# Kernel tuning notes

Measured on AMD Instinct MI355X. Metric: run time of the kernel, lower is better.

## Reference

```python
import jax, jax.numpy as jnp
import numpy as np

V, S, D, H, L, F = 32000, 1024, 1024, 16, 6, 4096
DH = D // H          # 64
HALF = DH // 2       # 32
EPS = 1e-5
ROPE_BASE = 10000.0


def setup_inputs() -> dict:
    key = jax.random.key(0)
    ks = jax.random.split(key, 16)
    std = 0.02
    inp = {
        "tokens": jax.random.randint(ks[0], (4, S), 0, V),
        "tok_emb": jax.random.normal(ks[1], (V, D), jnp.float32) * std,
        "ln1_s": jnp.ones((L, D), jnp.float32),
        "ln1_b": jnp.zeros((L, D), jnp.float32),
        "w_qkv": jax.random.normal(ks[2], (L, D, 3 * D), jnp.float32) * std,
        "w_proj": jax.random.normal(ks[3], (L, D, D), jnp.float32) * std,
        "ln2_s": jnp.ones((L, D), jnp.float32),
        "ln2_b": jnp.zeros((L, D), jnp.float32),
        "w_in": jax.random.normal(ks[4], (L, D, 2 * F), jnp.float32) * std,
        "w_out": jax.random.normal(ks[5], (L, F, D), jnp.float32) * std,
        "lnf_s": jnp.ones((D,), jnp.float32),
        "lnf_b": jnp.zeros((D,), jnp.float32),
        "w_score": jax.random.normal(ks[6], (D, 1), jnp.float32) * std,
        "w_cls": jax.random.normal(ks[7], (D, S), jnp.float32) * std,
    }
    return inp


def _layernorm(x, s, b):
    m = x.mean(-1, keepdims=True)
    v = ((x - m) ** 2).mean(-1, keepdims=True)
    return (x - m) * jax.lax.rsqrt(v + EPS) * s + b


def _rotate_half(x):
    x_even = x[..., ::2]
    x_odd = x[..., 1::2]
    return jnp.stack((-x_odd, x_even), axis=-1).reshape(x.shape)


def _rope_tables():
    inv_freq = 1.0 / (ROPE_BASE ** (jnp.arange(0, DH, 2, dtype=jnp.float32) / DH))
    pos = jnp.arange(S, dtype=jnp.float32)
    freqs = jnp.outer(pos, inv_freq)               # [S, DH/2]
    cos = jnp.repeat(jnp.cos(freqs), 2, axis=-1)   # [S, DH]
    sin = jnp.repeat(jnp.sin(freqs), 2, axis=-1)
    return cos, sin


def _forward(tokens, tok_emb, ln1_s, ln1_b, w_qkv, w_proj, ln2_s, ln2_b,
             w_in, w_out, lnf_s, lnf_b, w_score, w_cls):
    B = tokens.shape[0]
    cos, sin = _rope_tables()                      # [S, DH], broadcast over B,H
    lower = jnp.tril(jnp.ones((S, S), jnp.bool_))  # j <= i -> "down" subspace
    scale = HALF ** -0.5

    h = tok_emb[tokens]                            # [B, S, D]

    def block(h, p):
        l1s, l1b, Wqkv, Wp, l2s, l2b, Wi, Wo = p
        # --- dual-triangle attention ---
        qkv = _layernorm(h, l1s, l1b) @ Wqkv       # [B, S, 3D]
        q, k, v = jnp.split(qkv, 3, axis=-1)
        def heads(t):
            return t.reshape(B, S, H, DH).transpose(0, 2, 1, 3)  # [B,H,S,DH]
        q, k, v = heads(q), heads(k), heads(v)
        q = q * cos + _rotate_half(q) * sin
        k = k * cos + _rotate_half(k) * sin
        a_up = jnp.einsum('bhqd,bhkd->bhqk', q[..., :HALF], k[..., :HALF]) * scale
        a_dn = jnp.einsum('bhqd,bhkd->bhqk', q[..., HALF:], k[..., HALF:]) * scale
        logits = jnp.where(lower, a_dn, a_up)
        w = jax.nn.softmax(logits, axis=-1)
        o = jnp.einsum('bhqk,bhkd->bhqd', w, v)
        o = o.transpose(0, 2, 1, 3).reshape(B, S, D) @ Wp
        h = h + o
        # --- SwiGLU MLP ---
        g = _layernorm(h, l2s, l2b) @ Wi           # [B, S, 2F]
        a, b = jnp.split(g, 2, axis=-1)
        h = h + (jax.nn.silu(a) * b) @ Wo
        return h, None

    h, _ = jax.lax.scan(block, h, (ln1_s, ln1_b, w_qkv, w_proj, ln2_s, ln2_b, w_in, w_out))

    # pooling head: per-position scores -> softmax over positions -> weighted sum
    h = _layernorm(h, lnf_s, lnf_b)
    scores = h @ w_score                           # [B, S, 1]
    pw = jax.nn.softmax(scores, axis=1)
    pooled = jnp.sum(pw * h, axis=1)               # [B, D]
    return pooled @ w_cls                          # [B, S] logits over positions


def reference(tokens, tok_emb, ln1_s, ln1_b, w_qkv, w_proj, ln2_s, ln2_b,
              w_in, w_out, lnf_s, lnf_b, w_score, w_cls):
    return _forward(tokens, tok_emb, ln1_s, ln1_b, w_qkv, w_proj, ln2_s, ln2_b,
                    w_in, w_out, lnf_s, lnf_b, w_score, w_cls)
```

## Files before the change

kernel.cpp:

```cpp
#include <hip/hip_runtime.h>

#define Bsz 4
#define Ssz 1024
#define Dsz 1024
#define Hn  16
#define DHn 64
#define Ln  6
#define Fsz 4096
#define SCALE_ 0.1767766952966369f
#define LOG2E_ 1.4426950408889634f

typedef unsigned long long u64;
typedef __attribute__((ext_vector_type(8))) short bf16x8;
typedef __attribute__((ext_vector_type(4))) float f32x4;

__device__ __forceinline__ unsigned short f2bf(float f) {
  union { float f; unsigned int u; } v; v.f = f;
  unsigned int u = v.u + 0x7fffu + ((v.u >> 16) & 1u);
  return (unsigned short)(u >> 16);
}
__device__ __forceinline__ float bf2f(unsigned short h) {
  union { unsigned int u; float f; } v; v.u = ((unsigned int)h) << 16;
  return v.f;
}
__device__ __forceinline__ void gload_lds16(const void* g, void* lds) {
  __builtin_amdgcn_global_load_lds(
      (const __attribute__((address_space(1))) unsigned int*)g,
      (__attribute__((address_space(3))) unsigned int*)lds, 16, 0, 0);
}

__device__ __forceinline__ int swz_addr(int r, int lq) {
  int line = r >> 1;
  int u = ((r & 1) << 2) | lq;
  int s = u ^ (line & 7);
  return line * 128 + s * 16;
}

__device__ __forceinline__ bf16x8 frag_read(const char* base, int row, int lq) {
  return *(const bf16x8*)(base + row * 64 + ((lq ^ (row & 3)) * 16));
}

__global__ __launch_bounds__(256) void k_cossin(float* __restrict__ cosT, float* __restrict__ sinT) {
  int idx = blockIdx.x * 256 + threadIdx.x;
  if (idx >= Ssz * 32) return;
  int s = idx >> 5, i = idx & 31;
  float inv = powf(10000.f, -((float)(2 * i)) / 64.f);
  float f = (float)s * inv;
  cosT[idx] = cosf(f);
  sinT[idx] = sinf(f);
}

__global__ __launch_bounds__(256) void k_embed(const int* __restrict__ tokens,
                                               const float* __restrict__ emb,
                                               float* __restrict__ h) {
  int rs = blockIdx.x;
  int t = threadIdx.x;
  int tok = tokens[rs];
  *(float4*)&h[(u64)rs * Dsz + t * 4] = *(const float4*)&emb[(u64)tok * Dsz + t * 4];
}

template <int BF16OUT>
__global__ __launch_bounds__(256) void k_layernorm(const float* __restrict__ x,
                                                   const float* __restrict__ sc,
                                                   const float* __restrict__ bi,
                                                   void* outv) {
  int row = blockIdx.x, t = threadIdx.x;
  const float* xr = x + (u64)row * Dsz;
  float4 v = *(const float4*)&xr[t * 4];
  float sm = v.x + v.y + v.z + v.w;
  float sq = v.x * v.x + v.y * v.y + v.z * v.z + v.w * v.w;
#pragma unroll
  for (int m = 1; m < 64; m <<= 1) { sm += __shfl_xor(sm, m); sq += __shfl_xor(sq, m); }
  __shared__ float r1[4], r2[4];
  if ((t & 63) == 0) { r1[t >> 6] = sm; r2[t >> 6] = sq; }
  __syncthreads();
  sm = r1[0] + r1[1] + r1[2] + r1[3];
  sq = r2[0] + r2[1] + r2[2] + r2[3];
  float mean = sm * (1.f / Dsz);
  float inv = rsqrtf(sq * (1.f / Dsz) - mean * mean + 1e-5f);
  float4 s4 = *(const float4*)&sc[t * 4];
  float4 b4 = *(const float4*)&bi[t * 4];
  float y0 = (v.x - mean) * inv * s4.x + b4.x;
  float y1 = (v.y - mean) * inv * s4.y + b4.y;
  float y2 = (v.z - mean) * inv * s4.z + b4.z;
  float y3 = (v.w - mean) * inv * s4.w + b4.w;
  if (BF16OUT) {
    ushort4 o; o.x = f2bf(y0); o.y = f2bf(y1); o.z = f2bf(y2); o.w = f2bf(y3);
    *(ushort4*)((unsigned short*)outv + (u64)row * Dsz + t * 4) = o;
  } else {
    float4 o; o.x = y0; o.y = y1; o.z = y2; o.w = y3;
    *(float4*)((float*)outv + (u64)row * Dsz + t * 4) = o;
  }
}

#define PARTN 4194304ull
__global__ __launch_bounds__(256) void k_redres_ln(const float* __restrict__ p,
                                                   float* __restrict__ h,
                                                   const float* __restrict__ sc,
                                                   const float* __restrict__ bi,
                                                   unsigned short* __restrict__ xo) {
  int row = blockIdx.x, t = threadIdx.x;
  u64 base = (u64)row * Dsz + t * 4;
  float4 a = *(float4*)&h[base];
#pragma unroll
  for (int z = 0; z < 4; ++z) {
    float4 q = *(const float4*)&p[z * PARTN + base];
    a.x += q.x; a.y += q.y; a.z += q.z; a.w += q.w;
  }
  *(float4*)&h[base] = a;
  float sm = a.x + a.y + a.z + a.w;
  float sq = a.x * a.x + a.y * a.y + a.z * a.z + a.w * a.w;
#pragma unroll
  for (int m = 1; m < 64; m <<= 1) { sm += __shfl_xor(sm, m); sq += __shfl_xor(sq, m); }
  __shared__ float r1[4], r2[4];
  if ((t & 63) == 0) { r1[t >> 6] = sm; r2[t >> 6] = sq; }
  __syncthreads();
  sm = r1[0] + r1[1] + r1[2] + r1[3];
  sq = r2[0] + r2[1] + r2[2] + r2[3];
  float mean = sm * (1.f / Dsz);
  float inv = rsqrtf(sq * (1.f / Dsz) - mean * mean + 1e-5f);
  float4 s4 = *(const float4*)&sc[t * 4];
  float4 b4 = *(const float4*)&bi[t * 4];
  ushort4 o;
  o.x = f2bf((a.x - mean) * inv * s4.x + b4.x);
  o.y = f2bf((a.y - mean) * inv * s4.y + b4.y);
  o.z = f2bf((a.z - mean) * inv * s4.z + b4.z);
  o.w = f2bf((a.w - mean) * inv * s4.w + b4.w);
  *(ushort4*)&xo[base] = o;
}

__global__ __launch_bounds__(256) void k_redres(const float* __restrict__ p,
                                                float* __restrict__ h) {
  u64 i = ((u64)blockIdx.x * 256 + threadIdx.x) * 4;
  float4 a = *(float4*)&h[i];
#pragma unroll
  for (int z = 0; z < 4; ++z) {
    float4 q = *(const float4*)&p[z * PARTN + i];
    a.x += q.x; a.y += q.y; a.z += q.z; a.w += q.w;
  }
  *(float4*)&h[i] = a;
}

__global__ __launch_bounds__(256) void k_wt(const float* __restrict__ in,
                                            unsigned short* __restrict__ out, int K, int N) {
  in += (u64)blockIdx.z * K * N;
  out += (u64)blockIdx.z * K * N;
  __shared__ float tile[32][33];
  int nb = blockIdx.x * 32, kb = blockIdx.y * 32;
  int t = threadIdx.x;
  int r = t >> 3, c4 = (t & 7) * 4;
  float4 v = *(const float4*)&in[(u64)(kb + r) * N + nb + c4];
  tile[r][c4] = v.x; tile[r][c4 + 1] = v.y; tile[r][c4 + 2] = v.z; tile[r][c4 + 3] = v.w;
  __syncthreads();
  ushort4 o;
  o.x = f2bf(tile[c4][r]); o.y = f2bf(tile[c4 + 1][r]);
  o.z = f2bf(tile[c4 + 2][r]); o.w = f2bf(tile[c4 + 3][r]);
  *(ushort4*)&out[(u64)(nb + r) * K + kb + c4] = o;
}

__global__ __launch_bounds__(256) void k_wt_pair(const float* __restrict__ in,
                                                 unsigned short* __restrict__ out) {
  in += (u64)blockIdx.z * Dsz * 2 * Fsz;
  out += (u64)blockIdx.z * 2 * Fsz * Dsz;
  __shared__ float tile[32][33];
  int nb = blockIdx.x * 32, kb = blockIdx.y * 32;
  int t = threadIdx.x;
  int r = t >> 3, c4 = (t & 7) * 4;
  int s0 = nb >> 1;
  int srccol = (c4 < 16) ? (s0 + c4) : (Fsz + s0 + (c4 - 16));
  float4 v = *(const float4*)&in[(u64)(kb + r) * (2 * Fsz) + srccol];
  tile[r][c4] = v.x; tile[r][c4 + 1] = v.y; tile[r][c4 + 2] = v.z; tile[r][c4 + 3] = v.w;
  __syncthreads();
  int sc = (r >> 1) + (r & 1) * 16;
  ushort4 o;
  o.x = f2bf(tile[c4][sc]); o.y = f2bf(tile[c4 + 1][sc]);
  o.z = f2bf(tile[c4 + 2][sc]); o.w = f2bf(tile[c4 + 3][sc]);
  *(ushort4*)&out[(u64)(nb + r) * Dsz + kb + c4] = o;
}

template <int EPI>
__global__ __launch_bounds__(256, 3)
void k_ring(const unsigned short* __restrict__ A,
            const unsigned short* __restrict__ Bt,
            const float* resid, void* Cout,
            int M, int N, int K, int KH,
            unsigned short* qr, unsigned short* kr, unsigned short* vt,
            const float* cosT, const float* sinT) {
  __shared__ char lds[3][16384] __attribute__((aligned(16)));
  int t = threadIdx.x, w = t >> 6, l = t & 63;
  int wm = w >> 1, wn = w & 1;
  int lr = l & 15, lq = l >> 4;
  int bn = blockIdx.x, bm = blockIdx.y, kz = blockIdx.z;
  int NT = KH >> 5;
  int g0 = t, g1 = t + 256;
  int L0 = g0 >> 3, u0 = (g0 & 7) ^ (L0 & 7), row0 = 2 * L0 + (u0 >> 2), kc0 = (u0 & 3) * 8;
  int L1 = g1 >> 3, u1 = (g1 & 7) ^ (L1 & 7), row1 = 2 * L1 + (u1 >> 2), kc1 = (u1 & 3) * 8;
  const unsigned short* Az = A + (u64)kz * KH;
  const unsigned short* Bz = Bt + (u64)kz * KH;
  const char* Asrc0 = (const char*)(Az + (u64)(bm * 128 + row0) * K + kc0);
  const char* Asrc1 = (const char*)(Az + (u64)(bm * 128 + row1) * K + kc1);
  const char* Bsrc0 = (const char*)(Bz + (u64)(bn * 128 + row0) * K + kc0);
  const char* Bsrc1 = (const char*)(Bz + (u64)(bn * 128 + row1) * K + kc1);
  f32x4 acc[4][4];
#pragma unroll
  for (int i = 0; i < 4; ++i)
#pragma unroll
    for (int j = 0; j < 4; ++j) acc[i][j] = (f32x4){0.f, 0.f, 0.f, 0.f};
#define STG(slot, jj) { char* d_ = lds[slot]; \
    gload_lds16(Asrc0 + (u64)(jj) * 64, d_ + g0 * 16); \
    gload_lds16(Asrc1 + (u64)(jj) * 64, d_ + g1 * 16); \
    gload_lds16(Bsrc0 + (u64)(jj) * 64, d_ + 8192 + g0 * 16); \
    gload_lds16(Bsrc1 + (u64)(jj) * 64, d_ + 8192 + g1 * 16); }
  STG(0, 0); STG(1, 1);
  int cs = 0, ss = 2;
  for (int j = 0; j < NT; ++j) {
    if (j < NT - 1) asm volatile("s_waitcnt vmcnt(4)" ::: "memory");
    else            asm volatile("s_waitcnt vmcnt(0)" ::: "memory");
    __builtin_amdgcn_s_barrier();
    __builtin_amdgcn_sched_barrier(0);
    const char* Ab = lds[cs];
    const char* Bb = lds[cs] + 8192;
    if (j + 2 < NT) STG(ss, j + 2);
    bf16x8 afrag[4], bfrag[4];
#pragma unroll
    for (int ni = 0; ni < 4; ++ni)
      bfrag[ni] = *(const bf16x8*)(Bb + swz_addr(wn * 64 + ni * 16 + lr, lq));
#pragma unroll
    for (int mi = 0; mi < 4; ++mi)
      afrag[mi] = *(const bf16x8*)(Ab + swz_addr(wm * 64 + mi * 16 + lr, lq));
    __builtin_amdgcn_s_setprio(1);
#pragma unroll
    for (int mi = 0; mi < 4; ++mi)
#pragma unroll
      for (int ni = 0; ni < 4; ++ni)
        acc[mi][ni] = __builtin_amdgcn_mfma_f32_16x16x32_bf16(afrag[mi], bfrag[ni], acc[mi][ni], 0, 0, 0);
    __builtin_amdgcn_s_setprio(0);
    cs = (cs == 2) ? 0 : cs + 1;
    ss = (ss == 2) ? 0 : ss + 1;
  }
#undef STG
#pragma unroll
  for (int mi = 0; mi < 4; ++mi)
#pragma unroll
    for (int ni = 0; ni < 4; ++ni)
#pragma unroll
      for (int r = 0; r < 4; ++r) {
        int row = bm * 128 + wm * 64 + mi * 16 + lq * 4 + r;
        int col = bn * 128 + wn * 64 + ni * 16 + lr;
        float v = acc[mi][ni][r];
        if (EPI == 4) {
          float pv = __shfl_xor(v, 1);
          int b = row >> 10, s = row & 1023;
          int sec = col >> 10, c = col & 1023, hh = c >> 6, dh = c & 63;
          if (sec == 2) {
            vt[((u64)(b * Hn + hh) * DHn + dh) * Ssz + s] = f2bf(v);
          } else {
            int ci = s * 32 + (dh >> 1);
            float cs_ = cosT[ci], sn_ = sinT[ci];
            float out = (dh & 1) ? (v * cs_ + pv * sn_) : (v * cs_ - pv * sn_);
            u64 dst = ((u64)(b * Hn + hh) * Ssz + s) * DHn + dh;
            (sec == 0 ? qr : kr)[dst] = f2bf(out);
          }
        } else {
          u64 idx = (u64)row * N + col;
          if (EPI == 1) ((unsigned short*)Cout)[idx] = f2bf(v);
          else ((float*)Cout)[idx] = resid[idx] + v;
        }
      }
}

#define VM8 asm volatile("s_waitcnt vmcnt(8)" ::: "memory")
#define VM4 asm volatile("s_waitcnt vmcnt(4)" ::: "memory")
#define VM0 asm volatile("s_waitcnt vmcnt(0)" ::: "memory")
#define VMN

#define STGP(buf_, kh_, j_) { \
    char* dA = lds[buf_] + (kh_) * 16384; \
    char* dB = lds[buf_] + 32768 + (kh_) * 16384; \
    u64 ko = (u64)((j_) * 64 + (kh_) * 32) * 2; \
    gload_lds16(Ab0 + ko, dA + t * 16); \
    gload_lds16(Ab1 + ko, dA + 8192 + t * 16); \
    gload_lds16(Bb0 + ko, dB + t * 16); \
    gload_lds16(Bb1 + ko, dB + 8192 + t * 16); }

#define MFMA16(mibase) \
  _Pragma("unroll") for (int mi = 0; mi < 4; ++mi) \
    _Pragma("unroll") for (int ni = 0; ni < 4; ++ni) \
      acc[mi + (mibase)][ni] = __builtin_amdgcn_mfma_f32_16x16x32_bf16(afr[mi], bfr[ni], acc[mi + (mibase)][ni], 0, 0, 0);

#define PH_COMPUTE(mibase) \
  __builtin_amdgcn_s_barrier(); \
  asm volatile("s_waitcnt lgkmcnt(0)" ::: "memory"); \
  __builtin_amdgcn_sched_barrier(0); \
  __builtin_amdgcn_s_setprio(1); \
  MFMA16(mibase); \
  __builtin_amdgcn_s_setprio(0);

#define TILE256(jj, S1, S3, G1, G3) { \
  const int buf_ = (jj) & 1, kf_ = (jj) & 1, ks2_ = kf_ ^ 1; \
  const char* LA_ = lds[buf_]; \
  const char* LB_ = lds[buf_] + 32768; \
  bf16x8 afr[4], bfr[4]; \
   \
  _Pragma("unroll") for (int ni = 0; ni < 4; ++ni) \
    bfr[ni] = frag_read(LB_ + kf_ * 16384, wn * 64 + ni * 16 + lr, lq); \
  _Pragma("unroll") for (int mi = 0; mi < 4; ++mi) \
    afr[mi] = frag_read(LA_ + kf_ * 16384, wm * 128 + mi * 16 + lr, lq); \
  PH_COMPUTE(0); \
  __builtin_amdgcn_s_barrier(); \
   \
  _Pragma("unroll") for (int mi = 0; mi < 4; ++mi) \
    afr[mi] = frag_read(LA_ + kf_ * 16384, wm * 128 + (mi + 4) * 16 + lr, lq); \
  if (S1) STGP(buf_ ^ 1, kf_, (jj) + 1); \
  PH_COMPUTE(4); \
  G1; \
  __builtin_amdgcn_s_barrier(); \
   \
  _Pragma("unroll") for (int ni = 0; ni < 4; ++ni) \
    bfr[ni] = frag_read(LB_ + ks2_ * 16384, wn * 64 + ni * 16 + lr, lq); \
  _Pragma("unroll") for (int mi = 0; mi < 4; ++mi) \
    afr[mi] = frag_read(LA_ + ks2_ * 16384, wm * 128 + mi * 16 + lr, lq); \
  PH_COMPUTE(0); \
  __builtin_amdgcn_s_barrier(); \
   \
  _Pragma("unroll") for (int mi = 0; mi < 4; ++mi) \
    afr[mi] = frag_read(LA_ + ks2_ * 16384, wm * 128 + (mi + 4) * 16 + lr, lq); \
  if (S3) STGP(buf_, kf_, (jj) + 2); \
  PH_COMPUTE(4); \
  G3; \
  __builtin_amdgcn_s_barrier(); \
}

template <int EPI>
__global__ __launch_bounds__(512, 2)
void k_g256(const unsigned short* __restrict__ A,
            const unsigned short* __restrict__ Bt,
            void* Cout, int M, int N, int K, int KH) {
  __shared__ char lds[2][65536] __attribute__((aligned(16)));
  int t = threadIdx.x, w = t >> 6, l = t & 63;
  int wm = w >> 2, wn = w & 3;
  int lr = l & 15, lq = l >> 4;
  int bn = blockIdx.x, bm = blockIdx.y, kz = blockIdx.z;
  int NT = KH >> 6;
  int r0 = t >> 2, sl = t & 3;
  int c0 = (sl ^ (r0 & 3)) * 8;
  const unsigned short* Az = A + (u64)kz * KH;
  const unsigned short* Bz = Bt + (u64)kz * KH;
  const char* Ab0 = (const char*)(Az + (u64)(bm * 256 + r0) * K + c0);
  const char* Ab1 = (const char*)(Az + (u64)(bm * 256 + 128 + r0) * K + c0);
  const char* Bb0 = (const char*)(Bz + (u64)(bn * 256 + r0) * K + c0);
  const char* Bb1 = (const char*)(Bz + (u64)(bn * 256 + 128 + r0) * K + c0);
  f32x4 acc[8][4];
#pragma unroll
  for (int i = 0; i < 8; ++i)
#pragma unroll
    for (int j = 0; j < 4; ++j) acc[i][j] = (f32x4){0.f, 0.f, 0.f, 0.f};
  STGP(0, 0, 0);
  STGP(0, 1, 0);
  STGP(1, 1, 1);
  VM8;
  __builtin_amdgcn_s_barrier();
  for (int j = 0; j < NT - 2; ++j) TILE256(j, 1, 1, VM8, VM8);
  TILE256(NT - 2, 1, 0, VM8, VM4);
  TILE256(NT - 1, 0, 0, VM0, VMN);
  u64 zoff = (u64)kz * M * N;
#pragma unroll
  for (int mi = 0; mi < 8; ++mi)
#pragma unroll
    for (int ni = 0; ni < 4; ++ni)
#pragma unroll
      for (int r = 0; r < 4; ++r) {
        int row = bm * 256 + wm * 128 + mi * 16 + lq * 4 + r;
        int col = bn * 256 + wn * 64 + ni * 16 + lr;
        float v = acc[mi][ni][r];
        if (EPI == 3) {
          float pv = __shfl_xor(v, 1);
          if ((lr & 1) == 0) {
            float res = v / (1.f + __expf(-v)) * pv;
            ((unsigned short*)Cout)[(u64)row * (N >> 1) + (col >> 1)] = f2bf(res);
          }
        } else {
          ((float*)Cout)[zoff + (u64)row * N + col] = v;
        }
      }
}

__global__ __launch_bounds__(256) void k_attn(const unsigned short* __restrict__ qr,
                                              const unsigned short* __restrict__ kr,
                                              const unsigned short* __restrict__ vt,
                                              unsigned short* __restrict__ outp) {
  __shared__ unsigned short Klds[2][2][64 * 32] __attribute__((aligned(16)));
  __shared__ unsigned short Vlds[2][2][64 * 32] __attribute__((aligned(16)));
  __shared__ unsigned short Plds[4][16 * 64] __attribute__((aligned(16)));
  int qt = blockIdx.x, hh = blockIdx.y, b = blockIdx.z;
  int t = threadIdx.x, w = t >> 6, l = t & 63;
  int lr = l & 15, lq = l >> 4;
  u64 bh = (u64)(b * Hn + hh);
  const unsigned short* Qp = qr + bh * (Ssz * DHn);
  const unsigned short* Kp = kr + bh * (Ssz * DHn);
  const unsigned short* Vp = vt + bh * ((u64)DHn * Ssz);
  int q0 = qt * 64 + w * 16;
  bf16x8 qlo = *(const bf16x8*)&Qp[(q0 + lr) * DHn + lq * 8];
  bf16x8 qhi = *(const bf16x8*)&Qp[(q0 + lr) * DHn + 32 + lq * 8];
  int srow = t >> 2;
  int scol8 = (t & 3) * 8;
#define STAGEKV(bufi, kbase)                                                         \
  do {                                                                               \
    gload_lds16(&Kp[((kbase) + srow) * 64 + scol8],      (char*)&Klds[bufi][0][0] + t * 16); \
    gload_lds16(&Kp[((kbase) + srow) * 64 + 32 + scol8], (char*)&Klds[bufi][1][0] + t * 16); \
    gload_lds16(&Vp[(u64)srow * Ssz + (kbase) + scol8],      (char*)&Vlds[bufi][0][0] + t * 16); \
    gload_lds16(&Vp[(u64)srow * Ssz + (kbase) + 32 + scol8], (char*)&Vlds[bufi][1][0] + t * 16); \
  } while (0)
  float m_col = -1e30f, lsum = 0.f;
  float m_row[4] = {-1e30f, -1e30f, -1e30f, -1e30f};
  f32x4 o[4];
#pragma unroll
  for (int r = 0; r < 4; ++r) o[r] = (f32x4){0.f, 0.f, 0.f, 0.f};
  char* Pw = (char*)&Plds[w][0];

  STAGEKV(0, 0);
  asm volatile("s_waitcnt vmcnt(0)" ::: "memory");
  __syncthreads();
  int buf = 0;
  const float lsc = SCALE_ * LOG2E_;
  for (int kb = 0; kb < Ssz; kb += 64) {
    if (kb + 64 < Ssz) STAGEKV(buf ^ 1, kb + 64);
    float p[4][4];
#pragma unroll
    for (int ct = 0; ct < 4; ++ct) {
      int kc = kb + ct * 16;
      f32x4 z = (f32x4){0.f, 0.f, 0.f, 0.f};
      if (kc < q0) {
        bf16x8 khi = *(const bf16x8*)&Klds[buf][1][(ct * 16 + lr) * 32 + lq * 8];
        f32x4 shi = __builtin_amdgcn_mfma_f32_16x16x32_bf16(khi, qhi, z, 0, 0, 0);
#pragma unroll
        for (int r = 0; r < 4; ++r) p[ct][r] = shi[r] * lsc;
      } else if (kc > q0) {
        bf16x8 klo = *(const bf16x8*)&Klds[buf][0][(ct * 16 + lr) * 32 + lq * 8];
        f32x4 slo = __builtin_amdgcn_mfma_f32_16x16x32_bf16(klo, qlo, z, 0, 0, 0);
#pragma unroll
        for (int r = 0; r < 4; ++r) p[ct][r] = slo[r] * lsc;
      } else {
        bf16x8 klo = *(const bf16x8*)&Klds[buf][0][(ct * 16 + lr) * 32 + lq * 8];
        bf16x8 khi = *(const bf16x8*)&Klds[buf][1][(ct * 16 + lr) * 32 + lq * 8];
        f32x4 slo = __builtin_amdgcn_mfma_f32_16x16x32_bf16(klo, qlo, z, 0, 0, 0);
        f32x4 shi = __builtin_amdgcn_mfma_f32_16x16x32_bf16(khi, qhi, z, 0, 0, 0);
        int kg0 = kc + lq * 4;
        int qg = q0 + lr;
#pragma unroll
        for (int r = 0; r < 4; ++r) p[ct][r] = (kg0 + r <= qg ? shi[r] : slo[r]) * lsc;
      }
    }
    float tm = p[0][0];
#pragma unroll
    for (int ct = 0; ct < 4; ++ct)
#pragma unroll
      for (int r = 0; r < 4; ++r) tm = fmaxf(tm, p[ct][r]);
    tm = fmaxf(tm, __shfl_xor(tm, 16));
    tm = fmaxf(tm, __shfl_xor(tm, 32));
    if (__any(tm > m_col)) {
      float m_new = fmaxf(m_col, tm);
      lsum *= exp2f(m_col - m_new);
      m_col = m_new;
#pragma unroll
      for (int r = 0; r < 4; ++r) {
        float mr = __shfl(m_col, lq * 4 + r);
        float scf = exp2f(m_row[r] - mr);
        m_row[r] = mr;
        o[0][r] *= scf; o[1][r] *= scf; o[2][r] *= scf; o[3][r] *= scf;
      }
    }
#pragma unroll
    for (int ct = 0; ct < 4; ++ct) {
      float e0 = exp2f(p[ct][0] - m_col);
      float e1 = exp2f(p[ct][1] - m_col);
      float e2 = exp2f(p[ct][2] - m_col);
      float e3 = exp2f(p[ct][3] - m_col);
      lsum += e0 + e1 + e2 + e3;
      ushort4 pk; pk.x = f2bf(e0); pk.y = f2bf(e1); pk.z = f2bf(e2); pk.w = f2bf(e3);
      int byte_ = (lr * 128 + ct * 32 + lq * 8) ^ ((lr & 7) << 4);
      *(ushort4*)(Pw + byte_) = pk;
    }
    asm volatile("s_waitcnt lgkmcnt(0)" ::: "memory");
    __builtin_amdgcn_sched_barrier(0);
#pragma unroll
    for (int ks = 0; ks < 2; ++ks) {
      int pb = (lr * 128 + ks * 64 + lq * 16) ^ ((lr & 7) << 4);
      bf16x8 pa = *(const bf16x8*)(Pw + pb);
#pragma unroll
      for (int nt = 0; nt < 4; ++nt) {
        bf16x8 vb = *(const bf16x8*)&Vlds[buf][ks][(nt * 16 + lr) * 32 + lq * 8];
        o[nt] = __builtin_amdgcn_mfma_f32_16x16x32_bf16(pa, vb, o[nt], 0, 0, 0);
      }
    }
    asm volatile("s_waitcnt vmcnt(0)" ::: "memory");
    __syncthreads();
    buf ^= 1;
  }
  lsum += __shfl_xor(lsum, 16);
  lsum += __shfl_xor(lsum, 32);
  u64 obase = ((u64)b * Ssz) * Dsz + (u64)hh * DHn;
#pragma unroll
  for (int r = 0; r < 4; ++r) {
    float ls = __shfl(lsum, lq * 4 + r);
    float inv = 1.f / ls;
    int qrow = q0 + lq * 4 + r;
#pragma unroll
    for (int nt = 0; nt < 4; ++nt)
      outp[obase + (u64)qrow * Dsz + nt * 16 + lr] = f2bf(o[nt][r] * inv);
  }
#undef STAGEKV
}

__global__ __launch_bounds__(256) void k_scores(const float* __restrict__ hf,
                                                const float* __restrict__ wsc,
                                                float* __restrict__ scores) {
  int row = blockIdx.x * 4 + (threadIdx.x >> 6);
  int l = threadIdx.x & 63;
  const float* xr = hf + (u64)row * Dsz;
  float acc = 0.f;
#pragma unroll
  for (int j = 0; j < 4; ++j) {
    float4 v = *(const float4*)&xr[(j * 64 + l) * 4];
    float4 ww = *(const float4*)&wsc[(j * 64 + l) * 4];
    acc += v.x * ww.x + v.y * ww.y + v.z * ww.z + v.w * ww.w;
  }
#pragma unroll
  for (int m = 1; m < 64; m <<= 1) acc += __shfl_xor(acc, m);
  if (l == 0) scores[row] = acc;
}

__global__ __launch_bounds__(256) void k_softmax_s(const float* __restrict__ sc,
                                                   float* __restrict__ pw) {
  int b = blockIdx.x, t = threadIdx.x;
  const float* sr = sc + b * Ssz;
  float4 v = *(const float4*)&sr[t * 4];
  float mx = fmaxf(fmaxf(v.x, v.y), fmaxf(v.z, v.w));
#pragma unroll
  for (int m = 1; m < 64; m <<= 1) mx = fmaxf(mx, __shfl_xor(mx, m));
  __shared__ float red[4];
  if ((t & 63) == 0) red[t >> 6] = mx;
  __syncthreads();
  mx = fmaxf(fmaxf(red[0], red[1]), fmaxf(red[2], red[3]));
  float e0 = __expf(v.x - mx), e1 = __expf(v.y - mx), e2 = __expf(v.z - mx), e3 = __expf(v.w - mx);
  float sm = e0 + e1 + e2 + e3;
#pragma unroll
  for (int m = 1; m < 64; m <<= 1) sm += __shfl_xor(sm, m);
  __shared__ float red2[4];
  if ((t & 63) == 0) red2[t >> 6] = sm;
  __syncthreads();
  sm = red2[0] + red2[1] + red2[2] + red2[3];
  float inv = 1.f / sm;
  float4 o; o.x = e0 * inv; o.y = e1 * inv; o.z = e2 * inv; o.w = e3 * inv;
  *(float4*)&pw[b * Ssz + t * 4] = o;
}

__global__ __launch_bounds__(256) void k_pool1(const float* __restrict__ hf,
                                               const float* __restrict__ pw,
                                               float* __restrict__ part) {
  int d = blockIdx.x * 256 + threadIdx.x;
  int b = blockIdx.y, scn = blockIdx.z;
  const float* pwb = pw + b * Ssz + scn * 64;
  const float* hb = hf + ((u64)(b * Ssz + scn * 64)) * Dsz + d;
  float acc = 0.f;
#pragma unroll 4
  for (int s = 0; s < 64; ++s) acc += pwb[s] * hb[(u64)s * Dsz];
  part[(u64)(b * 16 + scn) * Dsz + d] = acc;
}
__global__ __launch_bounds__(256) void k_pool2(const float* __restrict__ part,
                                               float* __restrict__ pooled) {
  int d = blockIdx.x * 256 + threadIdx.x;
  int b = blockIdx.y;
  float acc = 0.f;
#pragma unroll
  for (int i = 0; i < 16; ++i) acc += part[(u64)(b * 16 + i) * Dsz + d];
  pooled[b * Dsz + d] = acc;
}

__global__ __launch_bounds__(256) void k_cls1(const float* __restrict__ pooled,
                                              const float* __restrict__ wcls,
                                              float* __restrict__ part) {
  int n = blockIdx.x * 64 + (threadIdx.x & 63);
  int b = threadIdx.x >> 6;
  int kz = blockIdx.y;
  const float* pb = pooled + b * Dsz + kz * 128;
  const float* wb = wcls + (u64)(kz * 128) * Ssz + n;
  float acc = 0.f;
#pragma unroll 4
  for (int k = 0; k < 128; ++k) acc += pb[k] * wb[(u64)k * Ssz];
  part[(u64)(kz * 4 + b) * Ssz + n] = acc;
}
__global__ __launch_bounds__(256) void k_cls2(const float* __restrict__ part,
                                              float* __restrict__ outp) {
  int n = blockIdx.x * 64 + (threadIdx.x & 63);
  int b = threadIdx.x >> 6;
  float acc = 0.f;
#pragma unroll
  for (int kz = 0; kz < 8; ++kz) acc += part[(u64)(kz * 4 + b) * Ssz + n];
  outp[b * Ssz + n] = acc;
}

extern "C" void kernel_launch(void* const* d_in, const int* in_sizes, int n_in,
                              void* d_out, int out_size, void* d_ws, size_t ws_size,
                              hipStream_t stream) {
  (void)in_sizes; (void)n_in; (void)out_size; (void)ws_size;
  const int*   tokens  = (const int*)  d_in[0];
  const float* tok_emb = (const float*)d_in[1];
  const float* ln1_s   = (const float*)d_in[2];
  const float* ln1_b   = (const float*)d_in[3];
  const float* w_qkv   = (const float*)d_in[4];
  const float* w_proj  = (const float*)d_in[5];
  const float* ln2_s   = (const float*)d_in[6];
  const float* ln2_b   = (const float*)d_in[7];
  const float* w_in    = (const float*)d_in[8];
  const float* w_out   = (const float*)d_in[9];
  const float* lnf_s   = (const float*)d_in[10];
  const float* lnf_b   = (const float*)d_in[11];
  const float* w_score = (const float*)d_in[12];
  const float* w_cls   = (const float*)d_in[13];
  float* outp = (float*)d_out;
  char* ws = (char*)d_ws;

  unsigned short* q_r    = (unsigned short*)(ws + 25165824ull);
  unsigned short* k_r    = (unsigned short*)(ws + 33554432ull);
  unsigned short* v_t    = (unsigned short*)(ws + 41943040ull);
  unsigned short* a_out  = (unsigned short*)(ws + 50331648ull);
  float*          hf     = (float*)(ws + 0);
  unsigned short* x_ln   = (unsigned short*)(ws + 67108864ull);
  unsigned short* mbuf   = (unsigned short*)(ws + 75497472ull);
  float*          h      = (float*)(ws + 109051904ull);
  float* cosT    = (float*)(ws + 125829120ull);
  float* sinT    = (float*)(ws + 125960192ull);
  float* scoresb = (float*)(ws + 126091264ull);
  float* pwb     = (float*)(ws + 126107648ull);
  float* pooledb = (float*)(ws + 126124032ull);
  float* poolpart= (float*)(ws + 126140416ull);
  float* clspart = (float*)(ws + 126402560ull);
  unsigned short* wqkv_t = (unsigned short*)(ws + 134217728ull);
  unsigned short* wproj_t= (unsigned short*)(ws + 171966464ull);
  unsigned short* win_t  = (unsigned short*)(ws + 184549376ull);
  unsigned short* wout_t = (unsigned short*)(ws + 285212672ull);
  float* skpart  = (float*)(ws + 335544320ull);

  dim3 blk(256);
  k_cossin<<<dim3(128), blk, 0, stream>>>(cosT, sinT);
  k_embed<<<dim3(4096), blk, 0, stream>>>(tokens, tok_emb, h);
  k_wt<<<dim3(96, 32, 6), blk, 0, stream>>>(w_qkv, wqkv_t, Dsz, 3 * Dsz);
  k_wt<<<dim3(32, 32, 6), blk, 0, stream>>>(w_proj, wproj_t, Dsz, Dsz);
  k_wt_pair<<<dim3(256, 32, 6), blk, 0, stream>>>(w_in, win_t);
  k_wt<<<dim3(32, 128, 6), blk, 0, stream>>>(w_out, wout_t, Fsz, Dsz);

  k_layernorm<1><<<dim3(4096), blk, 0, stream>>>(h, ln1_s, ln1_b, (void*)x_ln);
  for (int l = 0; l < Ln; ++l) {
    unsigned short* wq = wqkv_t + (u64)l * 3145728ull;
    unsigned short* wp = wproj_t + (u64)l * 1048576ull;
    unsigned short* wi = win_t + (u64)l * 8388608ull;
    unsigned short* wo = wout_t + (u64)l * 4194304ull;
    k_ring<4><<<dim3(24, 32), blk, 0, stream>>>(x_ln, wq, nullptr, nullptr,
        4096, 3072, 1024, 1024, q_r, k_r, v_t, cosT, sinT);
    k_attn<<<dim3(16, 16, 4), blk, 0, stream>>>(q_r, k_r, v_t, a_out);
    k_ring<2><<<dim3(8, 32), blk, 0, stream>>>(a_out, wp, h, (void*)h,
        4096, 1024, 1024, 1024, nullptr, nullptr, nullptr, nullptr, nullptr);
    k_layernorm<1><<<dim3(4096), blk, 0, stream>>>(h, ln2_s + l * Dsz, ln2_b + l * Dsz, (void*)x_ln);
    k_g256<3><<<dim3(32, 16), dim3(512), 0, stream>>>(x_ln, wi, (void*)mbuf, 4096, 8192, 1024, 1024);
    k_g256<0><<<dim3(4, 16, 4), dim3(512), 0, stream>>>(mbuf, wo, (void*)skpart, 4096, 1024, 4096, 1024);
    if (l < Ln - 1)
      k_redres_ln<<<dim3(4096), blk, 0, stream>>>(skpart, h,
          ln1_s + (l + 1) * Dsz, ln1_b + (l + 1) * Dsz, x_ln);
    else
      k_redres<<<dim3(4096), blk, 0, stream>>>(skpart, h);
  }

  k_layernorm<0><<<dim3(4096), blk, 0, stream>>>(h, lnf_s, lnf_b, (void*)hf);
  k_scores<<<dim3(1024), blk, 0, stream>>>(hf, w_score, scoresb);
  k_softmax_s<<<dim3(4), blk, 0, stream>>>(scoresb, pwb);
  k_pool1<<<dim3(4, 4, 16), blk, 0, stream>>>(hf, pwb, poolpart);
  k_pool2<<<dim3(4, 4), blk, 0, stream>>>(poolpart, pooledb);
  k_cls1<<<dim3(16, 8), blk, 0, stream>>>(pooledb, w_cls, clspart);
  k_cls2<<<dim3(16), blk, 0, stream>>>(clspart, outp);
}
```

Before: 1.943 ms.

## Swizzle GEMM blocks across XCDs and double attention query tile per block

GEMM kernels remap the flat block index so consecutive tiles land on the same XCD, which should improve L2 reuse of shared A/B panels. The attention kernel now uses 512 threads covering 128 queries per block, with K and V staging split between the two thread halves. Each staged K/V tile is therefore reused by twice as many query rows, halving K/V global traffic. The cost is fewer attention blocks, and occupancy may change. The XCD swizzle assumes the grid size is divisible by 8.

Result: faster. 1.892 ms (-2.6%).

```diff
diff --git a/kernel.cpp b/kernel.cpp
--- a/kernel.cpp
+++ b/kernel.cpp
@@ -38,6 +38,10 @@
 
 __device__ __forceinline__ bf16x8 frag_read(const char* base, int row, int lq) {
   return *(const bf16x8*)(base + row * 64 + ((lq ^ (row & 3)) * 16));
+}
+
+__device__ __forceinline__ int xcd_swz(int flat, int total) {
+  return (flat & 7) * (total >> 3) + (flat >> 3);
 }
 
 __global__ __launch_bounds__(256) void k_cossin(float* __restrict__ cosT, float* __restrict__ sinT) {
@@ -190,7 +194,11 @@
   int t = threadIdx.x, w = t >> 6, l = t & 63;
   int wm = w >> 1, wn = w & 1;
   int lr = l & 15, lq = l >> 4;
-  int bn = blockIdx.x, bm = blockIdx.y, kz = blockIdx.z;
+  int gx = gridDim.x;
+  int flat = blockIdx.y * gx + blockIdx.x;
+  int swzf = xcd_swz(flat, gx * gridDim.y);
+  int bm = swzf / gx, bn = swzf % gx;
+  int kz = blockIdx.z;
   int NT = KH >> 5;
   int g0 = t, g1 = t + 256;
   int L0 = g0 >> 3, u0 = (g0 & 7) ^ (L0 & 7), row0 = 2 * L0 + (u0 >> 2), kc0 = (u0 & 3) * 8;
@@ -301,28 +309,24 @@
   const char* LA_ = lds[buf_]; \
   const char* LB_ = lds[buf_] + 32768; \
   bf16x8 afr[4], bfr[4]; \
-   \
   _Pragma("unroll") for (int ni = 0; ni < 4; ++ni) \
     bfr[ni] = frag_read(LB_ + kf_ * 16384, wn * 64 + ni * 16 + lr, lq); \
   _Pragma("unroll") for (int mi = 0; mi < 4; ++mi) \
     afr[mi] = frag_read(LA_ + kf_ * 16384, wm * 128 + mi * 16 + lr, lq); \
   PH_COMPUTE(0); \
   __builtin_amdgcn_s_barrier(); \
-   \
   _Pragma("unroll") for (int mi = 0; mi < 4; ++mi) \
     afr[mi] = frag_read(LA_ + kf_ * 16384, wm * 128 + (mi + 4) * 16 + lr, lq); \
   if (S1) STGP(buf_ ^ 1, kf_, (jj) + 1); \
   PH_COMPUTE(4); \
   G1; \
   __builtin_amdgcn_s_barrier(); \
-   \
   _Pragma("unroll") for (int ni = 0; ni < 4; ++ni) \
     bfr[ni] = frag_read(LB_ + ks2_ * 16384, wn * 64 + ni * 16 + lr, lq); \
   _Pragma("unroll") for (int mi = 0; mi < 4; ++mi) \
     afr[mi] = frag_read(LA_ + ks2_ * 16384, wm * 128 + mi * 16 + lr, lq); \
   PH_COMPUTE(0); \
   __builtin_amdgcn_s_barrier(); \
-   \
   _Pragma("unroll") for (int mi = 0; mi < 4; ++mi) \
     afr[mi] = frag_read(LA_ + ks2_ * 16384, wm * 128 + (mi + 4) * 16 + lr, lq); \
   if (S3) STGP(buf_, kf_, (jj) + 2); \
@@ -340,7 +344,11 @@
   int t = threadIdx.x, w = t >> 6, l = t & 63;
   int wm = w >> 2, wn = w & 3;
   int lr = l & 15, lq = l >> 4;
-  int bn = blockIdx.x, bm = blockIdx.y, kz = blockIdx.z;
+  int gx = gridDim.x;
+  int flat = blockIdx.y * gx + blockIdx.x;
+  int swzf = xcd_swz(flat, gx * gridDim.y);
+  int bm = swzf / gx, bn = swzf % gx;
+  int kz = blockIdx.z;
   int NT = KH >> 6;
   int r0 = t >> 2, sl = t & 3;
   int c0 = (sl ^ (r0 & 3)) * 8;
@@ -385,13 +393,13 @@
       }
 }
 
-__global__ __launch_bounds__(256) void k_attn(const unsigned short* __restrict__ qr,
+__global__ __launch_bounds__(512) void k_attn(const unsigned short* __restrict__ qr,
                                               const unsigned short* __restrict__ kr,
                                               const unsigned short* __restrict__ vt,
                                               unsigned short* __restrict__ outp) {
   __shared__ unsigned short Klds[2][2][64 * 32] __attribute__((aligned(16)));
   __shared__ unsigned short Vlds[2][2][64 * 32] __attribute__((aligned(16)));
-  __shared__ unsigned short Plds[4][16 * 64] __attribute__((aligned(16)));
+  __shared__ unsigned short Plds[8][16 * 64] __attribute__((aligned(16)));
   int qt = blockIdx.x, hh = blockIdx.y, b = blockIdx.z;
   int t = threadIdx.x, w = t >> 6, l = t & 63;
   int lr = l & 15, lq = l >> 4;
@@ -399,17 +407,20 @@
   const unsigned short* Qp = qr + bh * (Ssz * DHn);
   const unsigned short* Kp = kr + bh * (Ssz * DHn);
   const unsigned short* Vp = vt + bh * ((u64)DHn * Ssz);
-  int q0 = qt * 64 + w * 16;
+  int q0 = qt * 128 + w * 16;
   bf16x8 qlo = *(const bf16x8*)&Qp[(q0 + lr) * DHn + lq * 8];
   bf16x8 qhi = *(const bf16x8*)&Qp[(q0 + lr) * DHn + 32 + lq * 8];
-  int srow = t >> 2;
-  int scol8 = (t & 3) * 8;
+  int u_ = t & 255;
+  int srow = u_ >> 2, scol8 = (u_ & 3) * 8;
 #define STAGEKV(bufi, kbase)                                                         \
   do {                                                                               \
-    gload_lds16(&Kp[((kbase) + srow) * 64 + scol8],      (char*)&Klds[bufi][0][0] + t * 16); \
-    gload_lds16(&Kp[((kbase) + srow) * 64 + 32 + scol8], (char*)&Klds[bufi][1][0] + t * 16); \
-    gload_lds16(&Vp[(u64)srow * Ssz + (kbase) + scol8],      (char*)&Vlds[bufi][0][0] + t * 16); \
-    gload_lds16(&Vp[(u64)srow * Ssz + (kbase) + 32 + scol8], (char*)&Vlds[bufi][1][0] + t * 16); \
+    if (t < 256) {                                                                   \
+      gload_lds16(&Kp[((kbase) + srow) * 64 + scol8],      (char*)&Klds[bufi][0][0] + u_ * 16); \
+      gload_lds16(&Kp[((kbase) + srow) * 64 + 32 + scol8], (char*)&Klds[bufi][1][0] + u_ * 16); \
+    } else {                                                                         \
+      gload_lds16(&Vp[(u64)srow * Ssz + (kbase) + scol8],      (char*)&Vlds[bufi][0][0] + u_ * 16); \
+      gload_lds16(&Vp[(u64)srow * Ssz + (kbase) + 32 + scol8], (char*)&Vlds[bufi][1][0] + u_ * 16); \
+    }                                                                                \
   } while (0)
   float m_col = -1e30f, lsum = 0.f;
   float m_row[4] = {-1e30f, -1e30f, -1e30f, -1e30f};
@@ -658,7 +669,7 @@
     unsigned short* wo = wout_t + (u64)l * 4194304ull;
     k_ring<4><<<dim3(24, 32), blk, 0, stream>>>(x_ln, wq, nullptr, nullptr,
         4096, 3072, 1024, 1024, q_r, k_r, v_t, cosT, sinT);
-    k_attn<<<dim3(16, 16, 4), blk, 0, stream>>>(q_r, k_r, v_t, a_out);
+    k_attn<<<dim3(8, 16, 4), dim3(512), 0, stream>>>(q_r, k_r, v_t, a_out);
     k_ring<2><<<dim3(8, 32), blk, 0, stream>>>(a_out, wp, h, (void*)h,
         4096, 1024, 1024, 1024, nullptr, nullptr, nullptr, nullptr, nullptr);
     k_layernorm<1><<<dim3(4096), blk, 0, stream>>>(h, ln2_s + l * Dsz, ln2_b + l * Dsz, (void*)x_ln);
```
